# Optimization experiments

Measured on AMD Instinct MI355X. Metric: run time of the kernel, lower is better.

## Reference

```python
import jax, jax.numpy as jnp
import numpy as np

H, HD, D = 16, 64, 1024
SCALE = HD ** -0.5
TEMP = 1.0
EPS = 1e-5

def setup_inputs() -> dict:
    key = jax.random.key(0)
    ks = jax.random.split(key, 10)
    B, N = 2, 2048
    lim = 1.0 / np.sqrt(D)
    def lin(k, out_d, in_d):
        k1, k2 = jax.random.split(k)
        W = jax.random.uniform(k1, (out_d, in_d), jnp.float32, -lim, lim)
        b = jax.random.uniform(k2, (out_d,), jnp.float32, -lim, lim)
        return W, b
    Wq, bq = lin(ks[0], H * HD, D)
    Wk, bk = lin(ks[1], H * HD, D)
    Wv, bv = lin(ks[2], H * HD, D)
    Wo, bo = lin(ks[3], D, H * HD)
    return {
        "x": jax.random.normal(ks[4], (B, N, D), jnp.float32),
        "adaptive_scale": jnp.ones((H,), jnp.float32),
        "Wq": Wq, "bq": bq, "Wk": Wk, "bk": bk, "Wv": Wv, "bv": bv,
        "Wo": Wo, "bo": bo,
        "gamma": jnp.ones((D,), jnp.float32),
        "beta": jnp.zeros((D,), jnp.float32),
    }

def reference(x, adaptive_scale, Wq, bq, Wk, bk, Wv, bv, Wo, bo, gamma, beta):
    B, N, _ = x.shape
    # self-attention: context = x
    Q = (x @ Wq.T + bq).reshape(B, N, H, HD)
    K = (x @ Wk.T + bk).reshape(B, N, H, HD)
    V = (x @ Wv.T + bv).reshape(B, N, H, HD)
    # per-head adaptive scale folded into scores (matches naive QK^T * scale / temp)
    scores = jnp.einsum('bnhd,bmhd->bhnm', Q, K)
    scores = scores * (SCALE * adaptive_scale)[None, :, None, None] / TEMP
    w = jax.nn.softmax(scores, axis=-1)  # [B,H,N,N]
    attn = jnp.einsum('bhnm,bmhd->bnhd', w, V).reshape(B, N, H * HD)
    y = x + (attn @ Wo.T + bo)
    mu = jnp.mean(y, axis=-1, keepdims=True)
    var = jnp.var(y, axis=-1, keepdims=True)
    return (y - mu) / jnp.sqrt(var + EPS) * gamma + beta
```

## Files before the change

kernel.cpp:

```cpp
#include <hip/hip_runtime.h>
#include <hip/hip_bf16.h>

using bf16 = __hip_bfloat16;
typedef __attribute__((ext_vector_type(8))) short short8;
typedef __attribute__((ext_vector_type(4))) short short4v;
typedef __attribute__((ext_vector_type(4))) float f32x4;

#define MFMA16(a, b, c) __builtin_amdgcn_mfma_f32_16x16x32_bf16((a), (b), (c), 0, 0, 0)

__device__ inline void async16(bf16* lds, const bf16* g) {
  __builtin_amdgcn_global_load_lds(
      (const __attribute__((address_space(1))) void*)g,
      (__attribute__((address_space(3))) void*)lds, 16, 0, 0);
}

__device__ inline short bfs(float x) {
  union { bf16 h; short s; } u; u.h = __float2bfloat16(x); return u.s;
}
__device__ inline short4v pack4(float a, float b, float c, float d) {
  short4v r; r[0] = bfs(a); r[1] = bfs(b); r[2] = bfs(c); r[3] = bfs(d); return r;
}
__device__ inline short4v pack4t(float a, float b, float c, float d) {
  unsigned lo = __builtin_amdgcn_perm(__float_as_uint(b), __float_as_uint(a), 0x07060302u);
  unsigned hi = __builtin_amdgcn_perm(__float_as_uint(d), __float_as_uint(c), 0x07060302u);
  union { unsigned u[2]; short4v v; } r;
  r.u[0] = lo; r.u[1] = hi;
  return r.v;
}

__global__ __launch_bounds__(256) void cvt_all(
    const float* __restrict__ x,  const float* __restrict__ Wq,
    const float* __restrict__ Wk, const float* __restrict__ Wv,
    const float* __restrict__ Wo,
    bf16* __restrict__ xb, bf16* __restrict__ Wqb, bf16* __restrict__ Wkb,
    bf16* __restrict__ Wvb, bf16* __restrict__ Wob) {
  int i = blockIdx.x * 256 + threadIdx.x;
  const float* s; bf16* d; int off;
  if (i < 1048576)      { s = x;  d = xb;  off = i; }
  else if (i < 1310720) { s = Wq; d = Wqb; off = i - 1048576; }
  else if (i < 1572864) { s = Wk; d = Wkb; off = i - 1310720; }
  else if (i < 1835008) { s = Wv; d = Wvb; off = i - 1572864; }
  else                  { s = Wo; d = Wob; off = i - 1835008; }
  float4 v = ((const float4*)s)[off];
  short4v o = pack4(v.x, v.y, v.z, v.w);
  *(short4v*)&d[(size_t)off * 4] = o;
}

__global__ __launch_bounds__(256) void gemm_qkv(
    const bf16* __restrict__ A,
    const bf16* __restrict__ Wq, const bf16* __restrict__ Wk, const bf16* __restrict__ Wv,
    const float* __restrict__ bq, const float* __restrict__ bk, const float* __restrict__ bv,
    const float* __restrict__ asc,
    bf16* __restrict__ Qb, bf16* __restrict__ Kb, bf16* __restrict__ Vtb) {
  __shared__ __align__(16) bf16 As[128 * 64];
  __shared__ __align__(16) bf16 Bs[128 * 64];
  __shared__ __align__(16) bf16 scrT[4][16 * 72];

  const int tid = threadIdx.x;
  const int lane = tid & 63;
  const int w = tid >> 6;
  const int m0 = blockIdx.x * 128;
  const int region = blockIdx.y >> 3;
  const int n0loc = (blockIdx.y & 7) * 128;
  const int wm = (w >> 1) * 64;
  const int wn = (w & 1) * 64;
  const int rq = lane & 15;
  const int quad = lane >> 4;

  const bf16* W = region == 0 ? Wq : (region == 1 ? Wk : Wv);
  const float* bias = region == 0 ? bq : (region == 1 ? bk : bv);
  bf16* C = region == 0 ? Qb : (region == 1 ? Kb : Vtb);

  f32x4 acc[4][4] = {};
  const bf16* Ag = A + (size_t)m0 * 1024;
  const bf16* Wg = W + (size_t)n0loc * 1024;

  const int srow = lane >> 3;
  const int sws = ((lane & 7) ^ srow) * 8;
  const int c0 = (quad ^ (rq & 7)) * 8;

  for (int k0 = 0; k0 < 1024; k0 += 64) {
    __syncthreads();
#pragma unroll
    for (int t = 0; t < 4; ++t) {
      int rb = w * 32 + t * 8;
      int row = rb + srow;
      async16(&As[rb * 64 + lane * 8], Ag + (size_t)row * 1024 + k0 + sws);
      async16(&Bs[rb * 64 + lane * 8], Wg + (size_t)row * 1024 + k0 + sws);
    }
    __syncthreads();

#pragma unroll
    for (int ks = 0; ks < 2; ++ks) {
      int off = c0 ^ (ks * 32);
      short8 a[4], b[4];
#pragma unroll
      for (int i = 0; i < 4; ++i) a[i] = *(const short8*)&As[(wm + i * 16 + rq) * 64 + off];
#pragma unroll
      for (int j = 0; j < 4; ++j) b[j] = *(const short8*)&Bs[(wn + j * 16 + rq) * 64 + off];
#pragma unroll
      for (int i = 0; i < 4; ++i)
#pragma unroll
        for (int j = 0; j < 4; ++j) acc[i][j] = MFMA16(a[i], b[j], acc[i][j]);
    }
  }

  const float LOG2E = 1.44269504088896f;
  if (region < 2) {
#pragma unroll
    for (int i = 0; i < 4; ++i)
#pragma unroll
      for (int j = 0; j < 4; ++j)
#pragma unroll
        for (int r2 = 0; r2 < 4; ++r2) {
          int m = m0 + wm + i * 16 + quad * 4 + r2;
          int nr = n0loc + wn + j * 16 + rq;
          int bb = m >> 11, t = m & 2047, h = nr >> 6, hd = nr & 63;
          float v = acc[i][j][r2] + bias[nr];
          if (region == 0) v *= 0.125f * asc[h] * LOG2E;
          C[(((size_t)(bb * 16 + h)) * 2048 + t) * 64 + hd] = __float2bfloat16(v);
        }
  } else {
    const int bb = m0 >> 11;
    const int h = (n0loc + wn) >> 6;
    const int tbase = (m0 & 2047) + wm;
    bf16* scr = scrT[w];
#pragma unroll
    for (int j = 0; j < 4; ++j) {
      int nr = n0loc + wn + j * 16 + rq;
      float bi = bias[nr];
#pragma unroll
      for (int i = 0; i < 4; ++i) {
        short4v pv = pack4(acc[i][j][0] + bi, acc[i][j][1] + bi,
                           acc[i][j][2] + bi, acc[i][j][3] + bi);
        *(short4v*)&scr[rq * 72 + i * 16 + quad * 4] = pv;
      }
#pragma unroll
      for (int pp = 0; pp < 4; ++pp) {
        int hdl = pp * 4 + quad;
        short4v v4 = *(const short4v*)&scr[hdl * 72 + rq * 4];
        size_t addr = (((size_t)(bb * 16 + h)) * 64 + j * 16 + hdl) * 2048 + tbase + rq * 4;
        *(short4v*)&C[addr] = v4;
      }
    }
  }
}

__global__ __launch_bounds__(256) void gemm_out(
    const bf16* __restrict__ A, const bf16* __restrict__ W,
    const float* __restrict__ bias, const float* __restrict__ R,
    float* __restrict__ Y) {
  __shared__ __align__(16) bf16 As[64 * 64];
  __shared__ __align__(16) bf16 Bs[128 * 64];

  const int tid = threadIdx.x;
  const int lane = tid & 63;
  const int w = tid >> 6;
  const int m0 = blockIdx.x * 64;
  const int n0 = blockIdx.y * 128;
  const int wm = (w >> 1) * 32;
  const int wn = (w & 1) * 64;
  const int rq = lane & 15;
  const int quad = lane >> 4;

  f32x4 acc[2][4] = {};
  const bf16* Ag = A + (size_t)m0 * 1024;
  const bf16* Wg = W + (size_t)n0 * 1024;

  const int srow = lane >> 3;
  const int sws = ((lane & 7) ^ srow) * 8;
  const int c0 = (quad ^ (rq & 7)) * 8;

  for (int k0 = 0; k0 < 1024; k0 += 64) {
    __syncthreads();
#pragma unroll
    for (int t = 0; t < 2; ++t) {
      int rb = w * 16 + t * 8;
      int row = rb + srow;
      async16(&As[rb * 64 + lane * 8], Ag + (size_t)row * 1024 + k0 + sws);
    }
#pragma unroll
    for (int t = 0; t < 4; ++t) {
      int rb = w * 32 + t * 8;
      int row = rb + srow;
      async16(&Bs[rb * 64 + lane * 8], Wg + (size_t)row * 1024 + k0 + sws);
    }
    __syncthreads();

#pragma unroll
    for (int ks = 0; ks < 2; ++ks) {
      int off = c0 ^ (ks * 32);
      short8 a[2], b[4];
#pragma unroll
      for (int i = 0; i < 2; ++i) a[i] = *(const short8*)&As[(wm + i * 16 + rq) * 64 + off];
#pragma unroll
      for (int j = 0; j < 4; ++j) b[j] = *(const short8*)&Bs[(wn + j * 16 + rq) * 64 + off];
#pragma unroll
      for (int i = 0; i < 2; ++i)
#pragma unroll
        for (int j = 0; j < 4; ++j) acc[i][j] = MFMA16(a[i], b[j], acc[i][j]);
    }
  }

#pragma unroll
  for (int i = 0; i < 2; ++i)
#pragma unroll
    for (int j = 0; j < 4; ++j)
#pragma unroll
      for (int r2 = 0; r2 < 4; ++r2) {
        int m = m0 + wm + i * 16 + quad * 4 + r2;
        int n = n0 + wn + j * 16 + rq;
        Y[(size_t)m * 1024 + n] = acc[i][j][r2] + bias[n] + R[(size_t)m * 1024 + n];
      }
}

#define LP 72
__global__ __launch_bounds__(256, 4) void attn_kernel(
    const bf16* __restrict__ Qb, const bf16* __restrict__ Kb,
    const bf16* __restrict__ Vtb,
    bf16* __restrict__ P0, bf16* __restrict__ P1, float* __restrict__ lbuf) {
  __shared__ __align__(16) bf16 Ks[64 * 64];
  __shared__ __align__(16) bf16 Vs[64 * 64];
  __shared__ __align__(16) bf16 Ps[4][32 * LP];

  const int q0 = blockIdx.x * 128;
  const int h = blockIdx.y;
  const int b = blockIdx.z & 1;
  const int half = blockIdx.z >> 1;
  const int tid = threadIdx.x;
  const int lane = tid & 63;
  const int w = tid >> 6;
  const int rq = lane & 15;
  const int quad = lane >> 4;
  const int kq = quad * 8;

  const size_t head = ((size_t)(b * 16 + h)) * 2048 * 64;
  const bf16* Qh = Qb + head;
  const bf16* Kh = Kb + head;
  const bf16* Vh = Vtb + head;

  short8 aq[2][2];
#pragma unroll
  for (int s = 0; s < 2; ++s) {
    const bf16* qrow = Qh + (size_t)(q0 + w * 32 + s * 16 + rq) * 64;
    aq[s][0] = *(const short8*)&qrow[kq];
    aq[s][1] = *(const short8*)&qrow[kq + 32];
  }

  short8 ones;
#pragma unroll
  for (int i = 0; i < 8; ++i) ones[i] = (short)0x3F80;

  const int srow = lane >> 3;
  const int swsV = ((lane & 7) ^ srow) * 8;
  const int c0 = (quad ^ (rq & 7)) * 8;
  const int c1 = c0 ^ 32;

  f32x4 accO[2][4] = {};
  f32x4 lacc[2] = {};

  const int kt0 = half * 16;
  for (int kt = kt0; kt < kt0 + 16; ++kt) {
    __syncthreads();
#pragma unroll
    for (int t = 0; t < 2; ++t) {
      int rb = w * 16 + t * 8;
      int row = rb + srow;
      int swsK = ((lane & 7) ^ ((row >> 2) & 7)) * 8;
      async16(&Ks[rb * 64 + lane * 8], Kh + (size_t)(kt * 64 + row) * 64 + swsK);
      async16(&Vs[rb * 64 + lane * 8], Vh + (size_t)row * 2048 + kt * 64 + swsV);
    }
    __syncthreads();

    short8 bk[4][2];
#pragma unroll
    for (int j = 0; j < 4; ++j) {
      const bf16* kr = &Ks[(rq * 4 + j) * 64];
      bk[j][0] = *(const short8*)&kr[c0];
      bk[j][1] = *(const short8*)&kr[c1];
    }

#pragma unroll
    for (int s = 0; s < 2; ++s) {
      f32x4 S[4] = {};
#pragma unroll
      for (int j = 0; j < 4; ++j) {
        S[j] = MFMA16(aq[s][0], bk[j][0], S[j]);
        S[j] = MFMA16(aq[s][1], bk[j][1], S[j]);
      }
#pragma unroll
      for (int r = 0; r < 4; ++r) {
        short4v pv = pack4t(exp2f(S[0][r]), exp2f(S[1][r]),
                            exp2f(S[2][r]), exp2f(S[3][r]));
        *(short4v*)&Ps[w][(s * 16 + quad * 4 + r) * LP + rq * 4] = pv;
      }
    }

    short8 bv[4][2];
#pragma unroll
    for (int dt = 0; dt < 4; ++dt) {
      const bf16* vr = &Vs[(dt * 16 + rq) * 64];
      bv[dt][0] = *(const short8*)&vr[c0];
      bv[dt][1] = *(const short8*)&vr[c1];
    }
#pragma unroll
    for (int s = 0; s < 2; ++s) {
      short8 ap0 = *(const short8*)&Ps[w][(s * 16 + rq) * LP + kq];
      short8 ap1 = *(const short8*)&Ps[w][(s * 16 + rq) * LP + kq + 32];
#pragma unroll
      for (int dt = 0; dt < 4; ++dt) {
        accO[s][dt] = MFMA16(ap0, bv[dt][0], accO[s][dt]);
        accO[s][dt] = MFMA16(ap1, bv[dt][1], accO[s][dt]);
      }
      lacc[s] = MFMA16(ap0, ones, lacc[s]);
      lacc[s] = MFMA16(ap1, ones, lacc[s]);
    }
  }

  bf16* Pout = half ? P1 : P0;
  float* lout = lbuf + half * 65536;
#pragma unroll
  for (int s = 0; s < 2; ++s) {
#pragma unroll
    for (int dt = 0; dt < 4; ++dt)
#pragma unroll
      for (int r = 0; r < 4; ++r) {
        int t = q0 + w * 32 + s * 16 + quad * 4 + r;
        int d = dt * 16 + rq;
        Pout[((size_t)(b * 2048 + t)) * 1024 + h * 64 + d] =
            __float2bfloat16(accO[s][dt][r]);
      }
    if (rq == 0) {
#pragma unroll
      for (int r = 0; r < 4; ++r) {
        int t = q0 + w * 32 + s * 16 + quad * 4 + r;
        lout[(b * 16 + h) * 2048 + t] = lacc[s][r];
      }
    }
  }
}

__global__ __launch_bounds__(256) void combine_kernel(
    bf16* __restrict__ P0, const bf16* __restrict__ P1,
    const float* __restrict__ lbuf) {
  const int row = blockIdx.x;
  const int tid = threadIdx.x;
  const int col = tid * 4;
  const int b = row >> 11, t = row & 2047;
  const int h = col >> 6;
  const float l = lbuf[(b * 16 + h) * 2048 + t] + lbuf[65536 + (b * 16 + h) * 2048 + t];
  const float rl = 1.f / l;
  size_t base = (size_t)row * 1024 + col;
  short4v p0 = *(const short4v*)&P0[base];
  short4v p1 = *(const short4v*)&P1[base];
  union { short s; bf16 h; } u;
  float v[4];
#pragma unroll
  for (int i = 0; i < 4; ++i) {
    u.s = p0[i]; float a = __bfloat162float(u.h);
    u.s = p1[i]; float c = __bfloat162float(u.h);
    v[i] = (a + c) * rl;
  }
  *(short4v*)&P0[base] = pack4(v[0], v[1], v[2], v[3]);
}

__global__ __launch_bounds__(256) void ln_kernel(
    const float* __restrict__ Y, const float* __restrict__ gamma,
    const float* __restrict__ beta, float* __restrict__ out) {
  const int row = blockIdx.x;
  const int tid = threadIdx.x;
  const int lane = tid & 63;
  const int w = tid >> 6;
  const float* y = Y + (size_t)row * 1024;

  float4 v = *(const float4*)&y[tid * 4];
  float s = v.x + v.y + v.z + v.w;
  float ss = v.x * v.x + v.y * v.y + v.z * v.z + v.w * v.w;
#pragma unroll
  for (int msk = 1; msk < 64; msk <<= 1) {
    s += __shfl_xor(s, msk);
    ss += __shfl_xor(ss, msk);
  }
  __shared__ float red[2][4];
  if (lane == 0) { red[0][w] = s; red[1][w] = ss; }
  __syncthreads();
  s = red[0][0] + red[0][1] + red[0][2] + red[0][3];
  ss = red[1][0] + red[1][1] + red[1][2] + red[1][3];
  float mean = s * (1.f / 1024.f);
  float var = ss * (1.f / 1024.f) - mean * mean;
  float rstd = rsqrtf(var + 1e-5f);
  float4 g = *(const float4*)&gamma[tid * 4];
  float4 bt = *(const float4*)&beta[tid * 4];
  float4 o;
  o.x = (v.x - mean) * rstd * g.x + bt.x;
  o.y = (v.y - mean) * rstd * g.y + bt.y;
  o.z = (v.z - mean) * rstd * g.z + bt.z;
  o.w = (v.w - mean) * rstd * g.w + bt.w;
  *(float4*)&out[(size_t)row * 1024 + tid * 4] = o;
}

extern "C" void kernel_launch(void* const* d_in, const int* in_sizes, int n_in,
                              void* d_out, int out_size, void* d_ws, size_t ws_size,
                              hipStream_t stream) {
  const float* x     = (const float*)d_in[0];
  const float* asc   = (const float*)d_in[1];
  const float* Wq    = (const float*)d_in[2];
  const float* bq    = (const float*)d_in[3];
  const float* Wk    = (const float*)d_in[4];
  const float* bk    = (const float*)d_in[5];
  const float* Wv    = (const float*)d_in[6];
  const float* bv    = (const float*)d_in[7];
  const float* Wo    = (const float*)d_in[8];
  const float* bo    = (const float*)d_in[9];
  const float* gamma = (const float*)d_in[10];
  const float* beta  = (const float*)d_in[11];
  float* out = (float*)d_out;

  char* ws = (char*)d_ws;
  const size_t MB = 1024 * 1024;
  bf16* Qb   = (bf16*)(ws);
  bf16* Kb   = (bf16*)(ws + 8 * MB);
  bf16* Vtb  = (bf16*)(ws + 16 * MB);
  bf16* attn = (bf16*)(ws + 24 * MB);
  bf16* xb   = (bf16*)(ws + 32 * MB);
  bf16* Wqb  = (bf16*)(ws + 40 * MB);
  bf16* Wkb  = (bf16*)(ws + 42 * MB);
  bf16* Wvb  = (bf16*)(ws + 44 * MB);
  bf16* Wob  = (bf16*)(ws + 46 * MB);
  float* y   = (float*)(ws);
  bf16* P1   = xb;
  float* lbuf = (float*)Wqb;

  cvt_all<<<dim3(8192), dim3(256), 0, stream>>>(x, Wq, Wk, Wv, Wo, xb, Wqb, Wkb, Wvb, Wob);
  gemm_qkv<<<dim3(32, 24), dim3(256), 0, stream>>>(xb, Wqb, Wkb, Wvb, bq, bk, bv, asc, Qb, Kb, Vtb);
  attn_kernel<<<dim3(16, 16, 4), dim3(256), 0, stream>>>(Qb, Kb, Vtb, attn, P1, lbuf);
  combine_kernel<<<dim3(4096), dim3(256), 0, stream>>>(attn, P1, lbuf);
  gemm_out<<<dim3(64, 8), dim3(256), 0, stream>>>(attn, Wob, bo, x, y);
  ln_kernel<<<dim3(4096), dim3(256), 0, stream>>>(y, gamma, beta, out);
}
```

Measured before the change: 219.8 us.

## Rewrite attention inner loop with 32x32 MFMA, register P transpose, double-buffered K/V

The attention kernel moves from 16x16x32 MFMA tiles to 32x32x16 tiles and computes S transposed (K as the A operand) so the exponentiated scores can be repacked into the P·V A-operand in registers with v_permlane32_swap. This removes the per-warp LDS staging buffer for P and its write/read round trip. K/V tiles are now double-buffered so the next tile's async load overlaps compute, with one barrier per iteration instead of two. The launch-bounds occupancy hint is dropped, and larger accumulators raise register pressure, which may lower occupancy.

```diff
diff --git a/kernel.cpp b/kernel.cpp
--- a/kernel.cpp
+++ b/kernel.cpp
@@ -5,8 +5,10 @@
 typedef __attribute__((ext_vector_type(8))) short short8;
 typedef __attribute__((ext_vector_type(4))) short short4v;
 typedef __attribute__((ext_vector_type(4))) float f32x4;
+typedef __attribute__((ext_vector_type(16))) float f32x16;
 
 #define MFMA16(a, b, c) __builtin_amdgcn_mfma_f32_16x16x32_bf16((a), (b), (c), 0, 0, 0)
+#define MFMA32(a, b, c) __builtin_amdgcn_mfma_f32_32x32x16_bf16((a), (b), (c), 0, 0, 0)
 
 __device__ inline void async16(bf16* lds, const bf16* g) {
   __builtin_amdgcn_global_load_lds(
@@ -26,6 +28,12 @@
   union { unsigned u[2]; short4v v; } r;
   r.u[0] = lo; r.u[1] = hi;
   return r.v;
+}
+__device__ inline unsigned pkt2(float x, float y) {
+  return __builtin_amdgcn_perm(__float_as_uint(y), __float_as_uint(x), 0x07060302u);
+}
+__device__ inline void pl32swap(unsigned& a, unsigned& b) {
+  asm("v_permlane32_swap_b32 %0, %1" : "+v"(a), "+v"(b));
 }
 
 __global__ __launch_bounds__(256) void cvt_all(
@@ -214,129 +222,121 @@
       }
 }
 
-#define LP 72
-__global__ __launch_bounds__(256, 4) void attn_kernel(
+__global__ __launch_bounds__(256) void attn_kernel(
     const bf16* __restrict__ Qb, const bf16* __restrict__ Kb,
     const bf16* __restrict__ Vtb,
     bf16* __restrict__ P0, bf16* __restrict__ P1, float* __restrict__ lbuf) {
-  __shared__ __align__(16) bf16 Ks[64 * 64];
-  __shared__ __align__(16) bf16 Vs[64 * 64];
-  __shared__ __align__(16) bf16 Ps[4][32 * LP];
+  __shared__ __align__(16) bf16 Ks[2][64 * 64];
+  __shared__ __align__(16) bf16 Vs[2][64 * 64];
 
   const int q0 = blockIdx.x * 128;
-  const int h = blockIdx.y;
+  const int hh = blockIdx.y;
   const int b = blockIdx.z & 1;
   const int half = blockIdx.z >> 1;
   const int tid = threadIdx.x;
   const int lane = tid & 63;
   const int w = tid >> 6;
-  const int rq = lane & 15;
-  const int quad = lane >> 4;
-  const int kq = quad * 8;
-
-  const size_t head = ((size_t)(b * 16 + h)) * 2048 * 64;
+  const int l31 = lane & 31;
+  const int hl = lane >> 5;
+  const int swz = l31 & 7;
+
+  const size_t head = ((size_t)(b * 16 + hh)) * 2048 * 64;
   const bf16* Qh = Qb + head;
   const bf16* Kh = Kb + head;
   const bf16* Vh = Vtb + head;
 
-  short8 aq[2][2];
-#pragma unroll
-  for (int s = 0; s < 2; ++s) {
-    const bf16* qrow = Qh + (size_t)(q0 + w * 32 + s * 16 + rq) * 64;
-    aq[s][0] = *(const short8*)&qrow[kq];
-    aq[s][1] = *(const short8*)&qrow[kq + 32];
-  }
+  short8 aq[4];
+#pragma unroll
+  for (int kc = 0; kc < 4; ++kc)
+    aq[kc] = *(const short8*)&Qh[(size_t)(q0 + w * 32 + l31) * 64 + kc * 16 + hl * 8];
 
   short8 ones;
 #pragma unroll
   for (int i = 0; i < 8; ++i) ones[i] = (short)0x3F80;
 
   const int srow = lane >> 3;
-  const int swsV = ((lane & 7) ^ srow) * 8;
-  const int c0 = (quad ^ (rq & 7)) * 8;
-  const int c1 = c0 ^ 32;
-
-  f32x4 accO[2][4] = {};
-  f32x4 lacc[2] = {};
+  const int sws = ((lane & 7) ^ srow) * 8;
+
+  f32x16 accO0 = {}, accO1 = {}, lacc = {};
 
   const int kt0 = half * 16;
-  for (int kt = kt0; kt < kt0 + 16; ++kt) {
-    __syncthreads();
+
+  auto stage = [&](int buf, int kt) {
 #pragma unroll
     for (int t = 0; t < 2; ++t) {
       int rb = w * 16 + t * 8;
       int row = rb + srow;
-      int swsK = ((lane & 7) ^ ((row >> 2) & 7)) * 8;
-      async16(&Ks[rb * 64 + lane * 8], Kh + (size_t)(kt * 64 + row) * 64 + swsK);
-      async16(&Vs[rb * 64 + lane * 8], Vh + (size_t)row * 2048 + kt * 64 + swsV);
-    }
+      async16(&Ks[buf][rb * 64 + lane * 8], Kh + (size_t)(kt * 64 + row) * 64 + sws);
+      async16(&Vs[buf][rb * 64 + lane * 8], Vh + (size_t)row * 2048 + kt * 64 + sws);
+    }
+  };
+
+  stage(0, kt0);
+  int cur = 0;
+  for (int kt = kt0; kt < kt0 + 16; ++kt) {
     __syncthreads();
-
-    short8 bk[4][2];
-#pragma unroll
-    for (int j = 0; j < 4; ++j) {
-      const bf16* kr = &Ks[(rq * 4 + j) * 64];
-      bk[j][0] = *(const short8*)&kr[c0];
-      bk[j][1] = *(const short8*)&kr[c1];
-    }
-
-#pragma unroll
-    for (int s = 0; s < 2; ++s) {
-      f32x4 S[4] = {};
-#pragma unroll
-      for (int j = 0; j < 4; ++j) {
-        S[j] = MFMA16(aq[s][0], bk[j][0], S[j]);
-        S[j] = MFMA16(aq[s][1], bk[j][1], S[j]);
-      }
-#pragma unroll
-      for (int r = 0; r < 4; ++r) {
-        short4v pv = pack4t(exp2f(S[0][r]), exp2f(S[1][r]),
-                            exp2f(S[2][r]), exp2f(S[3][r]));
-        *(short4v*)&Ps[w][(s * 16 + quad * 4 + r) * LP + rq * 4] = pv;
-      }
-    }
-
-    short8 bv[4][2];
-#pragma unroll
-    for (int dt = 0; dt < 4; ++dt) {
-      const bf16* vr = &Vs[(dt * 16 + rq) * 64];
-      bv[dt][0] = *(const short8*)&vr[c0];
-      bv[dt][1] = *(const short8*)&vr[c1];
-    }
-#pragma unroll
-    for (int s = 0; s < 2; ++s) {
-      short8 ap0 = *(const short8*)&Ps[w][(s * 16 + rq) * LP + kq];
-      short8 ap1 = *(const short8*)&Ps[w][(s * 16 + rq) * LP + kq + 32];
-#pragma unroll
-      for (int dt = 0; dt < 4; ++dt) {
-        accO[s][dt] = MFMA16(ap0, bv[dt][0], accO[s][dt]);
-        accO[s][dt] = MFMA16(ap1, bv[dt][1], accO[s][dt]);
-      }
-      lacc[s] = MFMA16(ap0, ones, lacc[s]);
-      lacc[s] = MFMA16(ap1, ones, lacc[s]);
-    }
+    if (kt + 1 < kt0 + 16) stage(cur ^ 1, kt + 1);
+
+    const bf16* Kc = Ks[cur];
+    const bf16* Vc = Vs[cur];
+
+    f32x16 S0 = {}, S1 = {};
+#pragma unroll
+    for (int kc = 0; kc < 4; ++kc) {
+      int co = (((kc << 1) | hl) ^ swz) * 8;
+      short8 k0 = *(const short8*)&Kc[l31 * 64 + co];
+      short8 k1 = *(const short8*)&Kc[(32 + l31) * 64 + co];
+      S0 = MFMA32(k0, aq[kc], S0);
+      S1 = MFMA32(k1, aq[kc], S1);
+    }
+#pragma unroll
+    for (int r = 0; r < 16; ++r) { S0[r] = exp2f(S0[r]); S1[r] = exp2f(S1[r]); }
+
+    short8 pa[4];
+#pragma unroll
+    for (int c = 0; c < 2; ++c) {
+      unsigned w0 = pkt2(S0[8 * c + 0], S0[8 * c + 1]);
+      unsigned w1 = pkt2(S0[8 * c + 2], S0[8 * c + 3]);
+      unsigned w2 = pkt2(S0[8 * c + 4], S0[8 * c + 5]);
+      unsigned w3 = pkt2(S0[8 * c + 6], S0[8 * c + 7]);
+      pl32swap(w0, w2); pl32swap(w1, w3);
+      union { unsigned u[4]; short8 v; } f;
+      f.u[0] = w0; f.u[1] = w1; f.u[2] = w2; f.u[3] = w3;
+      pa[c] = f.v;
+    }
+#pragma unroll
+    for (int c = 0; c < 2; ++c) {
+      unsigned w0 = pkt2(S1[8 * c + 0], S1[8 * c + 1]);
+      unsigned w1 = pkt2(S1[8 * c + 2], S1[8 * c + 3]);
+      unsigned w2 = pkt2(S1[8 * c + 4], S1[8 * c + 5]);
+      unsigned w3 = pkt2(S1[8 * c + 6], S1[8 * c + 7]);
+      pl32swap(w0, w2); pl32swap(w1, w3);
+      union { unsigned u[4]; short8 v; } f;
+      f.u[0] = w0; f.u[1] = w1; f.u[2] = w2; f.u[3] = w3;
+      pa[2 + c] = f.v;
+    }
+
+#pragma unroll
+    for (int cc = 0; cc < 4; ++cc) {
+      int co = (((cc << 1) | hl) ^ swz) * 8;
+      short8 v0 = *(const short8*)&Vc[l31 * 64 + co];
+      short8 v1 = *(const short8*)&Vc[(32 + l31) * 64 + co];
+      accO0 = MFMA32(pa[cc], v0, accO0);
+      accO1 = MFMA32(pa[cc], v1, accO1);
+      lacc = MFMA32(pa[cc], ones, lacc);
+    }
+    cur ^= 1;
   }
 
   bf16* Pout = half ? P1 : P0;
   float* lout = lbuf + half * 65536;
 #pragma unroll
-  for (int s = 0; s < 2; ++s) {
-#pragma unroll
-    for (int dt = 0; dt < 4; ++dt)
-#pragma unroll
-      for (int r = 0; r < 4; ++r) {
-        int t = q0 + w * 32 + s * 16 + quad * 4 + r;
-        int d = dt * 16 + rq;
-        Pout[((size_t)(b * 2048 + t)) * 1024 + h * 64 + d] =
-            __float2bfloat16(accO[s][dt][r]);
-      }
-    if (rq == 0) {
-#pragma unroll
-      for (int r = 0; r < 4; ++r) {
-        int t = q0 + w * 32 + s * 16 + quad * 4 + r;
-        lout[(b * 16 + h) * 2048 + t] = lacc[s][r];
-      }
-    }
+  for (int r = 0; r < 16; ++r) {
+    int t = q0 + w * 32 + (r & 3) + 8 * (r >> 2) + 4 * hl;
+    size_t base = ((size_t)(b * 2048 + t)) * 1024 + hh * 64;
+    Pout[base + l31]      = __float2bfloat16(accO0[r]);
+    Pout[base + 32 + l31] = __float2bfloat16(accO1[r]);
+    if (l31 == 0) lout[(b * 16 + hh) * 2048 + t] = lacc[r];
   }
 }
 
```

Result: slower. 238.9 us (+8.7%).

## Drop split-KV attention halves and combine kernel, normalize in-kernel with XCD-aware block remap

Applied to the files above, without the earlier changes.

The attention kernel no longer splits the key range into two halves. Each block now loops over all 32 key tiles and divides by the row sum before writing bf16 output, which removes the separate combine kernel and the partial-output and row-sum traffic it needed. Block IDs are remapped so that consecutive blocks dealt round-robin to the 8 XCDs share heads, which should improve L2 reuse of K and V. The launch-bounds occupancy hint drops from 4 to 2. The trade-off is half as many blocks (512) with twice the serial work each, so the GPU is less full.

```diff
diff --git a/kernel.cpp b/kernel.cpp
--- a/kernel.cpp
+++ b/kernel.cpp
@@ -215,18 +215,19 @@
 }
 
 #define LP 72
-__global__ __launch_bounds__(256, 4) void attn_kernel(
+__global__ __launch_bounds__(256, 2) void attn_kernel(
     const bf16* __restrict__ Qb, const bf16* __restrict__ Kb,
-    const bf16* __restrict__ Vtb,
-    bf16* __restrict__ P0, bf16* __restrict__ P1, float* __restrict__ lbuf) {
+    const bf16* __restrict__ Vtb, bf16* __restrict__ Pout) {
   __shared__ __align__(16) bf16 Ks[64 * 64];
   __shared__ __align__(16) bf16 Vs[64 * 64];
   __shared__ __align__(16) bf16 Ps[4][32 * LP];
 
-  const int q0 = blockIdx.x * 128;
-  const int h = blockIdx.y;
-  const int b = blockIdx.z & 1;
-  const int half = blockIdx.z >> 1;
+  const int wid = blockIdx.x + (blockIdx.y << 4) + (blockIdx.z << 8);
+  const int sid = (wid & 7) * 64 + (wid >> 3);
+  const int q0 = (sid & 15) * 128;
+  const int h = (sid >> 4) & 15;
+  const int b = sid >> 8;
+
   const int tid = threadIdx.x;
   const int lane = tid & 63;
   const int w = tid >> 6;
@@ -259,8 +260,7 @@
   f32x4 accO[2][4] = {};
   f32x4 lacc[2] = {};
 
-  const int kt0 = half * 16;
-  for (int kt = kt0; kt < kt0 + 16; ++kt) {
+  for (int kt = 0; kt < 32; ++kt) {
     __syncthreads();
 #pragma unroll
     for (int t = 0; t < 2; ++t) {
@@ -317,10 +317,11 @@
     }
   }
 
-  bf16* Pout = half ? P1 : P0;
-  float* lout = lbuf + half * 65536;
 #pragma unroll
   for (int s = 0; s < 2; ++s) {
+    f32x4 rl;
+#pragma unroll
+    for (int r = 0; r < 4; ++r) rl[r] = 1.f / lacc[s][r];
 #pragma unroll
     for (int dt = 0; dt < 4; ++dt)
 #pragma unroll
@@ -328,40 +329,9 @@
         int t = q0 + w * 32 + s * 16 + quad * 4 + r;
         int d = dt * 16 + rq;
         Pout[((size_t)(b * 2048 + t)) * 1024 + h * 64 + d] =
-            __float2bfloat16(accO[s][dt][r]);
-      }
-    if (rq == 0) {
-#pragma unroll
-      for (int r = 0; r < 4; ++r) {
-        int t = q0 + w * 32 + s * 16 + quad * 4 + r;
-        lout[(b * 16 + h) * 2048 + t] = lacc[s][r];
-      }
-    }
-  }
-}
-
-__global__ __launch_bounds__(256) void combine_kernel(
-    bf16* __restrict__ P0, const bf16* __restrict__ P1,
-    const float* __restrict__ lbuf) {
-  const int row = blockIdx.x;
-  const int tid = threadIdx.x;
-  const int col = tid * 4;
-  const int b = row >> 11, t = row & 2047;
-  const int h = col >> 6;
-  const float l = lbuf[(b * 16 + h) * 2048 + t] + lbuf[65536 + (b * 16 + h) * 2048 + t];
-  const float rl = 1.f / l;
-  size_t base = (size_t)row * 1024 + col;
-  short4v p0 = *(const short4v*)&P0[base];
-  short4v p1 = *(const short4v*)&P1[base];
-  union { short s; bf16 h; } u;
-  float v[4];
-#pragma unroll
-  for (int i = 0; i < 4; ++i) {
-    u.s = p0[i]; float a = __bfloat162float(u.h);
-    u.s = p1[i]; float c = __bfloat162float(u.h);
-    v[i] = (a + c) * rl;
-  }
-  *(short4v*)&P0[base] = pack4(v[0], v[1], v[2], v[3]);
+            __float2bfloat16(accO[s][dt][r] * rl[r]);
+      }
+  }
 }
 
 __global__ __launch_bounds__(256) void ln_kernel(
@@ -428,13 +398,10 @@
   bf16* Wvb  = (bf16*)(ws + 44 * MB);
   bf16* Wob  = (bf16*)(ws + 46 * MB);
   float* y   = (float*)(ws);
-  bf16* P1   = xb;
-  float* lbuf = (float*)Wqb;
 
   cvt_all<<<dim3(8192), dim3(256), 0, stream>>>(x, Wq, Wk, Wv, Wo, xb, Wqb, Wkb, Wvb, Wob);
   gemm_qkv<<<dim3(32, 24), dim3(256), 0, stream>>>(xb, Wqb, Wkb, Wvb, bq, bk, bv, asc, Qb, Kb, Vtb);
-  attn_kernel<<<dim3(16, 16, 4), dim3(256), 0, stream>>>(Qb, Kb, Vtb, attn, P1, lbuf);
-  combine_kernel<<<dim3(4096), dim3(256), 0, stream>>>(attn, P1, lbuf);
+  attn_kernel<<<dim3(16, 16, 2), dim3(256), 0, stream>>>(Qb, Kb, Vtb, attn);
   gemm_out<<<dim3(64, 8), dim3(256), 0, stream>>>(attn, Wob, bo, x, y);
   ln_kernel<<<dim3(4096), dim3(256), 0, stream>>>(y, gamma, beta, out);
 }
```

Measured after the change: 220.5 us. Within noise of the previous version (+0.3%).
